# Kernel tuning notes

Measured on AMD Instinct MI355X. Metric: run time of the kernel, lower is better.

Reference implementation:

```python
import jax, jax.numpy as jnp
import numpy as np

N = 512    # nnodes
H = 8      # attention heads
C = 32     # gnn_repr_size (per head)
ER = 32    # edge_repr_size
FE = 3     # feat_emb_size
E = 16384  # edges (avg degree 32)


def gat_conv(x, edge_index, edge_attr, W, att_src, att_dst, We, att_edge, b):
    """PyG GATConv (edge_dim=1, concat=True, add_self_loops=True, eval mode)."""
    n = x.shape[0]
    h_, c_ = att_src.shape
    row, col = edge_index[0], edge_index[1]
    # self loops with fill_value='mean': mean of incoming edge_attr per target node
    deg = jax.ops.segment_sum(jnp.ones_like(edge_attr), col, num_segments=n)
    loop_attr = jax.ops.segment_sum(edge_attr, col, num_segments=n) / jnp.maximum(deg, 1.0)
    ar = jnp.arange(n)
    row = jnp.concatenate([row, ar])
    col = jnp.concatenate([col, ar])
    ea = jnp.concatenate([edge_attr, loop_attr])
    # node projections [n, H, C]
    h = (x @ W.T).reshape(n, h_, c_)
    a_src = jnp.sum(h * att_src, axis=-1)  # [n, H]
    a_dst = jnp.sum(h * att_dst, axis=-1)  # [n, H]
    e = (ea[:, None] @ We.T).reshape(-1, h_, c_)  # [E', H, C]
    a_e = jnp.sum(e * att_edge, axis=-1)          # [E', H]
    alpha = jax.nn.leaky_relu(a_src[row] + a_dst[col] + a_e, 0.2)
    # softmax over edges grouped by destination node
    amax = jax.ops.segment_max(alpha, col, num_segments=n)
    ex = jnp.exp(alpha - amax[col])
    denom = jax.ops.segment_sum(ex, col, num_segments=n)
    alpha = ex / (denom[col] + 1e-16)
    out = jax.ops.segment_sum(h[row] * alpha[..., None], col, num_segments=n)
    return out.reshape(n, h_ * c_) + b


def setup_inputs():
    key = jax.random.key(0)
    ks = jax.random.split(key, 24)
    s = 0.05
    HC = H * C
    in_len = N * ER + 3 * N + 3 * FE  # combiner1 input length
    return {
        "dist": jax.random.uniform(ks[0], (N, N), dtype=jnp.float32),
        "markov": jax.random.uniform(ks[1], (N, N), dtype=jnp.float32),
        "demand": jax.random.normal(ks[2], (N,), dtype=jnp.float32),
        "W_week": jax.random.normal(ks[3], (7, FE)) * s,
        "W_cap": jax.random.normal(ks[4], (26, FE)) * s,
        "W_veh": jax.random.normal(ks[5], (15, FE)) * s,
        "g1_W": jax.random.normal(ks[6], (HC, 1)) * s,
        "g1_att_src": jax.random.normal(ks[7], (H, C)) * s,
        "g1_att_dst": jax.random.normal(ks[8], (H, C)) * s,
        "g1_We": jax.random.normal(ks[9], (HC, 1)) * s,
        "g1_att_edge": jax.random.normal(ks[10], (H, C)) * s,
        "g1_b": jnp.zeros((HC,), dtype=jnp.float32),
        "g2_W": jax.random.normal(ks[11], (HC, HC)) * s,
        "g2_att_src": jax.random.normal(ks[12], (H, C)) * s,
        "g2_att_dst": jax.random.normal(ks[13], (H, C)) * s,
        "g2_We": jax.random.normal(ks[14], (HC, 1)) * s,
        "g2_att_edge": jax.random.normal(ks[15], (H, C)) * s,
        "g2_b": jnp.zeros((HC,), dtype=jnp.float32),
        "Wes": jax.random.normal(ks[16], (ER, 2 * HC)) * s,
        "bes": jnp.zeros((ER,), dtype=jnp.float32),
        "Wc1": jax.random.normal(ks[17], (N, in_len)) * 0.01,
        "bc1": jnp.zeros((N,), dtype=jnp.float32),
        "Wc2": jax.random.normal(ks[18], (N, N)) * s,
        "bc2": jnp.zeros((N,), dtype=jnp.float32),
        "stops": jax.random.randint(ks[19], (256,), 0, N),
        "edge_index": jax.random.randint(ks[20], (2, E), 0, N),
        "weekday": 3,
        "vehicles": 7,
        "capacity": 12,
    }


def reference(dist, markov, demand, W_week, W_cap, W_veh,
              g1_W, g1_att_src, g1_att_dst, g1_We, g1_att_edge, g1_b,
              g2_W, g2_att_src, g2_att_dst, g2_We, g2_att_edge, g2_b,
              Wes, bes, Wc1, bc1, Wc2, bc2,
              stops, edge_index, weekday, vehicles, capacity):
    n = dist.shape[0]
    dist = (dist - dist.min()) / (dist.max() - dist.min())
    x = demand[:, None]  # [n, 1]
    ea = markov[edge_index[0], edge_index[1]]  # [E]
    x = jax.nn.relu(gat_conv(x, edge_index, ea, g1_W, g1_att_src, g1_att_dst, g1_We, g1_att_edge, g1_b))
    x = jax.nn.relu(gat_conv(x, edge_index, ea, g2_W, g2_att_src, g2_att_dst, g2_We, g2_att_edge, g2_b))
    HC_ = x.shape[1]
    # all-pairs edge representation: concat(x[i], x[j]) over meshgrid -> [n*n, 2*HC]
    er = jnp.concatenate([
        jnp.broadcast_to(x[:, None, :], (n, n, HC_)),
        jnp.broadcast_to(x[None, :, :], (n, n, HC_)),
    ], axis=-1).reshape(n * n, 2 * HC_)
    er = (er @ Wes.T + bes).reshape(n, -1)  # [n, n*ER]
    week = jnp.broadcast_to(W_week[weekday], (n, W_week.shape[1]))
    cap = jnp.broadcast_to(W_cap[capacity], (n, W_cap.shape[1]))
    veh = jnp.broadcast_to(W_veh[vehicles], (n, W_veh.shape[1]))
    stop = jnp.broadcast_to(jnp.zeros((n,), dtype=dist.dtype).at[stops].set(1.0)[None, :], (n, n))
    feat = jnp.concatenate([er, dist, markov, week, cap, veh, stop], axis=1)
    out = jax.nn.relu(feat @ Wc1.T + bc1) @ Wc2.T + bc2
    return out
```

## Files before the change

### kernel.cpp

```cpp
#include <hip/hip_runtime.h>
#include <hip/hip_bf16.h>

typedef __hip_bfloat16 bf16;
typedef __attribute__((ext_vector_type(8))) short bf16x8;
typedef __attribute__((ext_vector_type(4))) float f32x4;

#define NNODE 512
#define NEDGE 16384
#define INLEN 17929
#define K1P   1088

#define WS_EA      0
#define WS_CSRC    16384
#define WS_CEA     32768
#define WS_DEG     49152
#define WS_STARTS  49664
#define WS_LATTR   50176
#define WS_MM      50688
#define WS_MMP     50690
#define WS_STOPV   50818
#define WS_AE      51330
#define WS_PS      51346
#define WS_H       55552
#define WS_G2WT    186624
#define WS_H2      317696
#define WS_ASRC    448768
#define WS_ADST    452864
#define WS_UV      456960
#define WS_K       489728
#define WS_APACK   490240
#define WS_BPACK   768768
#define WS_OUT1    1047296
#define WS_WC2B    1178368
#define WS_WESF    1309440
#define WS_ASRC2   1325824
#define WS_ADST2   1329920
#define WS_CURSOR  1334016
#define WS_DEGP    1334528
#define WS_LSUMP   1367296

static __device__ __forceinline__ unsigned short f2bfbits(float x){
  bf16 b = __float2bfloat16(x);
  union { bf16 b; unsigned short u; } c; c.b = b; return c.u;
}

__global__ __launch_bounds__(256)
void k_prep(const float* __restrict__ demand, const float* __restrict__ W1,
            const float* __restrict__ att_s, const float* __restrict__ att_d,
            const int* __restrict__ stops, const float* __restrict__ Wes,
            const float* __restrict__ dist, const float* __restrict__ markov,
            const int* __restrict__ eidx,
            const float* __restrict__ g1We, const float* __restrict__ g1ae,
            const float* __restrict__ g2We, const float* __restrict__ g2ae,
            const float* __restrict__ g2W,  const float* __restrict__ g2as,
            const float* __restrict__ g2ad, const float* __restrict__ Wc2,
            float* ws){
  int b = blockIdx.x, tid = threadIdx.x;
  if (b < 512){
    int hd = tid>>5, c = tid&31;
    float hv = demand[b] * W1[tid];
    ws[WS_H + b*256 + tid] = hv;
    float ps = hv * att_s[tid];
    float pd = hv * att_d[tid];
    for (int off=16; off; off>>=1){ ps += __shfl_down(ps,off,32); pd += __shfl_down(pd,off,32); }
    if (c==0){ ws[WS_ASRC + b*8+hd]=ps; ws[WS_ADST + b*8+hd]=pd; }
  } else if (b == 512){
    ws[WS_STOPV+tid] = 0.f; ws[WS_STOPV+256+tid] = 0.f;
    __syncthreads();
    ws[WS_STOPV + stops[tid]] = 1.0f;
    if (tid < 8){
      float s=0.f; for (int c=0;c<32;c++) s += g1We[tid*32+c]*g1ae[tid*32+c];
      ws[WS_AE+tid]=s;
    } else if (tid < 16){
      int h=tid-8; float s=0.f; for (int c=0;c<32;c++) s += g2We[h*32+c]*g2ae[h*32+c];
      ws[WS_AE+8+h]=s;
    }
  } else if (b < 515){
    for (int idx = (b-513)*8192 + tid; idx < (b-512)*8192; idx += 256){
      int k = idx>>8, c = idx&255;
      ws[WS_WESF+idx] = (k<32) ? Wes[k*512+c] : Wes[(k-32)*512+256+c];
    }
  } else if (b < 579){
    __shared__ float smn[256], smx[256];
    int p = b-515;
    float mn = 3.4e38f, mx = -3.4e38f;
    const float4* dv = (const float4*)(dist + p*4096);
    #pragma unroll
    for (int k=0;k<4;k++){
      float4 v = dv[k*256 + tid];
      mn = fminf(mn, fminf(fminf(v.x,v.y), fminf(v.z,v.w)));
      mx = fmaxf(mx, fmaxf(fmaxf(v.x,v.y), fmaxf(v.z,v.w)));
    }
    smn[tid]=mn; smx[tid]=mx; __syncthreads();
    for (int off=128; off; off>>=1){
      if (tid<off){ smn[tid]=fminf(smn[tid],smn[tid+off]); smx[tid]=fmaxf(smx[tid],smx[tid+off]); }
      __syncthreads();
    }
    if (tid==0){ ws[WS_MMP+p]=smn[0]; ws[WS_MMP+64+p]=smx[0]; }
  } else if (b < 643){
    __shared__ int   hd_[512];
    __shared__ float hf_[512];
    int k = b-579;
    hd_[tid]=0; hd_[256+tid]=0; hf_[tid]=0.f; hf_[256+tid]=0.f;
    __syncthreads();
    int e = k*256 + tid;
    int r = eidx[e], c = eidx[NEDGE+e];
    float a = markov[r*NNODE + c];
    ws[WS_EA+e] = a;
    atomicAdd(&hd_[c], 1);
    atomicAdd(&hf_[c], a);
    __syncthreads();
    ((int*)(ws+WS_DEGP))[k*512+tid]     = hd_[tid];
    ((int*)(ws+WS_DEGP))[k*512+256+tid] = hd_[256+tid];
    ws[WS_LSUMP + k*512+tid]     = hf_[tid];
    ws[WS_LSUMP + k*512+256+tid] = hf_[256+tid];
  } else if (b < 659){
    int j = b-643;
    const float* att = (j<8) ? g2as : g2ad;
    int h = j&7;
    float s = 0.f;
    for (int c=0;c<32;c++) s += att[h*32+c] * g2W[(h*32+c)*256 + tid];
    ws[WS_PS + j*256 + tid] = s;
  } else if (b < 675){
    __shared__ float T[64][65];
    int tb = b-659, tr = tb>>2, tc = tb&3;
    int w = tid>>6, c = tid&63;
    for (int k=0;k<16;k++){
      int r = k*4 + w;
      T[r][c] = g2W[(tr*64+r)*256 + tc*64 + c];
    }
    __syncthreads();
    for (int k=0;k<16;k++){
      int r = k*4 + w;
      ws[WS_G2WT + (tc*64+r)*256 + tr*64 + c] = T[c][r];
    }
  } else if (b == 675){
    ((int*)(ws+WS_CURSOR))[tid] = 0;
    ((int*)(ws+WS_CURSOR))[256+tid] = 0;
  } else {
    int blk = b - 676;
    const float4* src = (const float4*)(Wc2 + blk*4096);
    ushort4* dst = (ushort4*)((unsigned short*)(ws+WS_WC2B) + blk*4096);
    #pragma unroll
    for (int i=0;i<4;i++){
      float4 v = src[i*256+tid];
      ushort4 u;
      u.x = f2bfbits(v.x); u.y = f2bfbits(v.y);
      u.z = f2bfbits(v.z); u.w = f2bfbits(v.w);
      dst[i*256+tid] = u;
    }
  }
}

__global__ __launch_bounds__(512)
void k_scansc(const int* __restrict__ eidx, float* ws){
  __shared__ int sc[512];
  __shared__ int startS[512];
  __shared__ float rmn[64], rmx[64];
  int t = threadIdx.x, b = blockIdx.x;
  const int* dp = (const int*)(ws+WS_DEGP);
  int d = 0;
  for (int k=0;k<64;k++) d += dp[k*512+t];
  sc[t] = d; __syncthreads();
  for (int off=1; off<512; off<<=1){
    int v = (t>=off) ? sc[t-off] : 0; __syncthreads();
    sc[t] += v; __syncthreads();
  }
  startS[t] = sc[t]-d;
  if (b == 0){
    float l = 0.f;
    for (int k=0;k<64;k++) l += ws[WS_LSUMP+k*512+t];
    ((int*)(ws+WS_STARTS))[t] = startS[t];
    ((int*)(ws+WS_DEG))[t] = d;
    ws[WS_LATTR+t] = l / (float)(d>1 ? d : 1);
    if (t < 64){ rmn[t]=ws[WS_MMP+t]; rmx[t]=ws[WS_MMP+64+t]; }
    __syncthreads();
    if (t == 0){
      float mn=rmn[0], mx=rmx[0];
      for (int i=1;i<64;i++){ mn=fminf(mn,rmn[i]); mx=fmaxf(mx,rmx[i]); }
      ws[WS_MM]=mn; ws[WS_MM+1]=mx;
    }
  }
  __syncthreads();
  int e = b*512 + t;
  int c = eidx[NEDGE+e];
  int p = startS[c] + atomicAdd((int*)(ws+WS_CURSOR)+c, 1);
  ((int*)(ws+WS_CSRC))[p] = eidx[e];
  ws[WS_CEA+p] = ws[WS_EA+e];
}

template<int MODE>
__global__ __launch_bounds__(256)
void k_agg(const float* __restrict__ hbuf, const float* __restrict__ asrc,
           const float* __restrict__ adst, const int* __restrict__ csrc,
           const float* __restrict__ cea, const int* __restrict__ starts,
           const int* __restrict__ deg, const float* __restrict__ lattr,
           const float* __restrict__ AEp, const float* __restrict__ bvec,
           const float* __restrict__ dist, const float* __restrict__ markov,
           float* ws){
  int t = blockIdx.x, tid = threadIdx.x, hd = tid>>5;
  __shared__ int   srcE[256];
  __shared__ float eaE[256];
  __shared__ float Lall[256*8];
  __shared__ float AE[8], mh[8], dh[8], sw[8];
  __shared__ float xrow[256], uvrow[64];
  if (tid<8) AE[tid]=AEp[tid];
  __syncthreads();
  int d = deg[t], s0 = starts[t];
  if (d > 256) d = 256;
  for (int e=tid; e<d; e+=256){ srcE[e]=csrc[s0+e]; eaE[e]=cea[s0+e]; }
  __syncthreads();
  {
    int h8 = tid&7;
    float adt = adst[t*8+h8], aeh = AE[h8];
    for (int e = tid>>3; e < d; e += 32){
      float a = asrc[srcE[e]*8+h8] + adt + eaE[e]*aeh;
      Lall[e*8+h8] = a>=0.f ? a : 0.2f*a;
    }
  }
  __syncthreads();
  {
    int h = tid>>5, j = tid&31;
    float aself = asrc[t*8+h] + adst[t*8+h] + lattr[t]*AE[h];
    aself = aself>=0.f ? aself : 0.2f*aself;
    float mm = aself;
    for (int e=j; e<d; e+=32) mm = fmaxf(mm, Lall[e*8+h]);
    for (int off=16; off; off>>=1) mm = fmaxf(mm, __shfl_down(mm,off,32));
    mm = __shfl(mm, 0, 32);
    float dd = 0.f;
    for (int e=j; e<d; e+=32) dd += __expf(Lall[e*8+h]-mm);
    for (int off=16; off; off>>=1) dd += __shfl_down(dd,off,32);
    if (j==0){
      float se = __expf(aself-mm);
      mh[h]=mm; dh[h]=dd+se+1e-16f; sw[h]=se;
    }
  }
  __syncthreads();
  {
    int h8 = tid&7;
    for (int e = tid>>3; e < d; e += 32)
      Lall[e*8+h8] = __expf(Lall[e*8+h8] - mh[h8]);
  }
  __syncthreads();
  float a0 = sw[hd]*hbuf[t*256+tid], a1=0.f, a2=0.f, a3=0.f;
  int e = 0;
  for (; e+4<=d; e+=4){
    a0 += Lall[(e+0)*8+hd]*hbuf[srcE[e+0]*256+tid];
    a1 += Lall[(e+1)*8+hd]*hbuf[srcE[e+1]*256+tid];
    a2 += Lall[(e+2)*8+hd]*hbuf[srcE[e+2]*256+tid];
    a3 += Lall[(e+3)*8+hd]*hbuf[srcE[e+3]*256+tid];
  }
  for (; e<d; e++) a0 += Lall[e*8+hd]*hbuf[srcE[e]*256+tid];
  float v = fmaxf(((a0+a1)+(a2+a3))/dh[hd] + bvec[tid], 0.f);
  xrow[tid] = v;
  __syncthreads();
  if (MODE == 1){
    const float* g2wt = ws + WS_G2WT;
    float h0=0.f,h1=0.f,h2=0.f,h3=0.f;
    for (int c=0;c<256;c+=4){
      h0 += xrow[c+0]*g2wt[(c+0)*256+tid];
      h1 += xrow[c+1]*g2wt[(c+1)*256+tid];
      h2 += xrow[c+2]*g2wt[(c+2)*256+tid];
      h3 += xrow[c+3]*g2wt[(c+3)*256+tid];
    }
    ws[WS_H2 + t*256 + tid] = (h0+h1)+(h2+h3);
    if (tid < 64){
      int j = tid>>2, q = tid&3;
      const float* pr = ws + WS_PS + j*256 + q*64;
      const float* xr = xrow + q*64;
      float p = 0.f;
      for (int c=0;c<64;c++) p += xr[c]*pr[c];
      p += __shfl_down(p,2,4);
      p += __shfl_down(p,1,4);
      if (q==0){
        if (j<8) ws[WS_ASRC2 + t*8+j] = p;
        else     ws[WS_ADST2 + t*8+(j-8)] = p;
      }
    }
  } else {
    int k = tid>>2, q = tid&3;
    const float* wr = ws + WS_WESF + k*256 + q*64;
    const float* xr = xrow + q*64;
    float p = 0.f;
    for (int c=0;c<64;c++) p += xr[c]*wr[c];
    p += __shfl_down(p,2,4);
    p += __shfl_down(p,1,4);
    if (q==0){ ws[WS_UV + t*64+k] = p; uvrow[k] = p; }
    __syncthreads();
    float mn = ws[WS_MM], mx = ws[WS_MM+1];
    float inv = 1.0f/(mx-mn);
    bf16* ap = (bf16*)(ws+WS_APACK);
    const float* mrow = markov + t*512;
    for (int j=tid; j<K1P; j+=256){
      float v2;
      if (j<32)        v2 = uvrow[j];
      else if (j<544)  v2 = (dist[t*512 + j-32] - mn) * inv;
      else if (j<1056) v2 = mrow[j-544];
      else             v2 = 0.f;
      ap[(size_t)t*K1P + j] = __float2bfloat16(v2);
    }
  }
}

__global__ __launch_bounds__(1024)
void k_skpack(const float* __restrict__ Wc1, const float* __restrict__ bc1,
              const float* __restrict__ bes, const float* __restrict__ Wweek,
              const float* __restrict__ Wcap, const float* __restrict__ Wveh,
              const int* __restrict__ wd, const int* __restrict__ vh,
              const int* __restrict__ cp, float* ws){
  int o = blockIdx.x, tid = threadIdx.x;
  __shared__ float besf[32];
  __shared__ float red[512];
  __shared__ float red2[16];
  if (tid<32) besf[tid] = bes[tid];
  __syncthreads();
  const float* wr = Wc1 + (size_t)o*INLEN;
  bf16* bp  = (bf16*)(ws+WS_BPACK);
  float be = besf[tid&31];
  const float* uvp = ws + WS_UV + ((tid>>5)<<6) + 32 + (tid&31);
  float sP = 0.f, tP0=0.f, tP1=0.f, tP2=0.f, tP3=0.f;
  #pragma unroll
  for (int i=0;i<16;i+=4){
    float w0 = wr[tid + 1024*(i+0)];
    float w1 = wr[tid + 1024*(i+1)];
    float w2 = wr[tid + 1024*(i+2)];
    float w3 = wr[tid + 1024*(i+3)];
    float u0 = uvp[2048*(i+0)];
    float u1 = uvp[2048*(i+1)];
    float u2 = uvp[2048*(i+2)];
    float u3 = uvp[2048*(i+3)];
    sP += (w0+w1)+(w2+w3);
    tP0 += w0*(u0+be);
    tP1 += w1*(u1+be);
    tP2 += w2*(u2+be);
    tP3 += w3*(u3+be);
  }
  float tP = (tP0+tP1)+(tP2+tP3);
  if (tid < 512) tP += ws[WS_STOPV+tid] * wr[17417+tid];
  if (tid < 9){
    int g = tid/3, f = tid-g*3;
    float sv = (g==0) ? Wweek[wd[0]*3+f]
             : (g==1) ? Wcap[cp[0]*3+f]
                      : Wveh[vh[0]*3+f];
    tP += sv * wr[17408+tid];
  }
  int lane = tid&63, w = tid>>6;
  sP += __shfl_down(sP, 32, 64);
  if (lane < 32) red[w*32 + lane] = sP;
  for (int off=32; off; off>>=1) tP += __shfl_down(tP, off, 64);
  if (lane == 0) red2[w] = tP;
  __syncthreads();
  if (tid < 32){
    float s = 0.f;
    #pragma unroll
    for (int k=0;k<16;k++) s += red[k*32+tid];
    bp[(size_t)o*K1P + tid] = __float2bfloat16(s);
    bp[(size_t)o*K1P + 1056 + tid] = __float2bfloat16(0.f);
  } else if (tid == 32){
    float s = 0.f;
    #pragma unroll
    for (int k=0;k<16;k++) s += red2[k];
    ws[WS_K+o] = s + bc1[o];
  }
  bp[(size_t)o*K1P + 32 + tid] = __float2bfloat16(wr[16384+tid]);
}

template<bool RELU, bool BF16OUT>
__global__ __launch_bounds__(512)
void gemm_mfma(const bf16* __restrict__ A, const bf16* __restrict__ B,
               const float* __restrict__ bias, float* __restrict__ Cf,
               bf16* __restrict__ Cb, int M, int N, int K){
  __shared__ short Als[2][4096];
  __shared__ short Bls[2][4096];
  const int tid = threadIdx.x;
  const int bm = blockIdx.y*64, bn = blockIdx.x*64;
  const int wave = tid>>6, lane = tid&63;
  const int wm = wave>>2, wn = wave&3;
  const int r = lane&15, q = lane>>4;
  f32x4 acc[2] = {};
  const int lrow = tid>>3, lk8 = tid&7;
  const bf16* Ag = A + (size_t)(bm+lrow)*K + lk8*8;
  const bf16* Bg = B + (size_t)(bn+lrow)*K + lk8*8;
  const int sidx = ((lk8>>2)*256 + (lk8&3)*64 + lrow)*8;
  const int nk = K>>6;
  float4 av = *(const float4*)(Ag);
  float4 bv = *(const float4*)(Bg);
  *(float4*)(&Als[0][sidx]) = av;
  *(float4*)(&Bls[0][sidx]) = bv;
  __syncthreads();
  for (int kk=0; kk<nk; kk++){
    int cur = kk&1, nxt = cur^1;
    if (kk+1 < nk){
      av = *(const float4*)(Ag + (kk+1)*64);
      bv = *(const float4*)(Bg + (kk+1)*64);
    }
    #pragma unroll
    for (int kk2=0; kk2<2; kk2++){
      bf16x8 bfr = *(const bf16x8*)(&Bls[cur][(kk2*256 + q*64 + wn*16 + r)*8]);
      #pragma unroll
      for (int i=0;i<2;i++){
        bf16x8 af = *(const bf16x8*)(&Als[cur][(kk2*256 + q*64 + wm*32 + i*16 + r)*8]);
        acc[i] = __builtin_amdgcn_mfma_f32_16x16x32_bf16(af, bfr, acc[i], 0,0,0);
      }
    }
    if (kk+1 < nk){
      __syncthreads();
      *(float4*)(&Als[nxt][sidx]) = av;
      *(float4*)(&Bls[nxt][sidx]) = bv;
      __syncthreads();
    }
  }
  #pragma unroll
  for (int i=0;i<2;i++){
    int row = bm + wm*32 + i*16 + q*4;
    int col = bn + wn*16 + r;
    float bi = bias ? bias[col] : 0.f;
    #pragma unroll
    for (int g=0; g<4; g++){
      float v = acc[i][g] + bi;
      if (RELU) v = fmaxf(v, 0.f);
      if (BF16OUT) Cb[(size_t)(row+g)*N + col] = __float2bfloat16(v);
      else         Cf[(size_t)(row+g)*N + col] = v;
    }
  }
}

extern "C" void kernel_launch(void* const* d_in, const int* in_sizes, int n_in,
                              void* d_out, int out_size, void* d_ws, size_t ws_size,
                              hipStream_t stream){
  const float* dist   = (const float*)d_in[0];
  const float* markov = (const float*)d_in[1];
  const float* demand = (const float*)d_in[2];
  const float* Wweek  = (const float*)d_in[3];
  const float* Wcap   = (const float*)d_in[4];
  const float* Wveh   = (const float*)d_in[5];
  const float* g1W    = (const float*)d_in[6];
  const float* g1as   = (const float*)d_in[7];
  const float* g1ad   = (const float*)d_in[8];
  const float* g1We   = (const float*)d_in[9];
  const float* g1ae   = (const float*)d_in[10];
  const float* g1b    = (const float*)d_in[11];
  const float* g2W    = (const float*)d_in[12];
  const float* g2as   = (const float*)d_in[13];
  const float* g2ad   = (const float*)d_in[14];
  const float* g2We   = (const float*)d_in[15];
  const float* g2ae   = (const float*)d_in[16];
  const float* g2b    = (const float*)d_in[17];
  const float* Wes    = (const float*)d_in[18];
  const float* bes    = (const float*)d_in[19];
  const float* Wc1    = (const float*)d_in[20];
  const float* bc1    = (const float*)d_in[21];
  const float* Wc2    = (const float*)d_in[22];
  const float* bc2    = (const float*)d_in[23];
  const int*   stops  = (const int*)d_in[24];
  const int*   eidx   = (const int*)d_in[25];
  const int*   wd     = (const int*)d_in[26];
  const int*   vh     = (const int*)d_in[27];
  const int*   cp     = (const int*)d_in[28];
  float* out = (float*)d_out;
  float* ws = (float*)d_ws;

  const int*   csrc   = (const int*)(ws+WS_CSRC);
  const float* cea    = ws+WS_CEA;
  const int*   starts = (const int*)(ws+WS_STARTS);
  const int*   deg    = (const int*)(ws+WS_DEG);
  const float* lattr  = ws+WS_LATTR;

  k_prep<<<740,256,0,stream>>>(demand, g1W, g1as, g1ad, stops, Wes, dist, markov, eidx,
                               g1We, g1ae, g2We, g2ae, g2W, g2as, g2ad, Wc2, ws);
  k_scansc<<<32,512,0,stream>>>(eidx, ws);
  k_agg<1><<<512,256,0,stream>>>(ws+WS_H, ws+WS_ASRC, ws+WS_ADST, csrc, cea, starts, deg,
                                 lattr, ws+WS_AE, g1b, dist, markov, ws);
  k_agg<2><<<512,256,0,stream>>>(ws+WS_H2, ws+WS_ASRC2, ws+WS_ADST2, csrc, cea, starts, deg,
                                 lattr, ws+WS_AE+8, g2b, dist, markov, ws);
  k_skpack<<<512,1024,0,stream>>>(Wc1, bc1, bes, Wweek, Wcap, Wveh, wd, vh, cp, ws);
  gemm_mfma<true,true><<<dim3(8,8),512,0,stream>>>((const bf16*)(ws+WS_APACK), (const bf16*)(ws+WS_BPACK),
                                                   ws+WS_K, nullptr, (bf16*)(ws+WS_OUT1), 512, 512, K1P);
  gemm_mfma<false,false><<<dim3(8,8),512,0,stream>>>((const bf16*)(ws+WS_OUT1), (const bf16*)(ws+WS_WC2B),
                                                     bc2, out, nullptr, 512, 512, 512);
}
```

Measured before the change: 204.4 us.

## Fuse all stages into one cooperative persistent kernel with grid syncs

Merges the seven separate launches (prep, scan/scatter, two aggregation passes, skpack, two GEMMs) into a single cooperative kernel of 512 blocks of 256 threads. Stages are separated by grid.sync(), and their shared memory is overlaid in a union. The aim is to remove per-launch overhead and the gaps between kernels. In exchange, the skpack and GEMM stages are reshaped to 256-thread blocks: skpack gets a longer per-thread loop, and the GEMMs run on only 64 blocks while the rest sit idle. Each grid barrier costs time, and the whole grid must fit co-resident.

```diff
diff --git a/kernel.cpp b/kernel.cpp
--- a/kernel.cpp
+++ b/kernel.cpp
@@ -1,5 +1,8 @@
 #include <hip/hip_runtime.h>
 #include <hip/hip_bf16.h>
+#include <hip/hip_cooperative_groups.h>
+
+namespace cg = cooperative_groups;
 
 typedef __hip_bfloat16 bf16;
 typedef __attribute__((ext_vector_type(8))) short bf16x8;
@@ -44,27 +47,276 @@
   union { bf16 b; unsigned short u; } c; c.b = b; return c.u;
 }
 
-__global__ __launch_bounds__(256)
-void k_prep(const float* __restrict__ demand, const float* __restrict__ W1,
-            const float* __restrict__ att_s, const float* __restrict__ att_d,
-            const int* __restrict__ stops, const float* __restrict__ Wes,
-            const float* __restrict__ dist, const float* __restrict__ markov,
-            const int* __restrict__ eidx,
-            const float* __restrict__ g1We, const float* __restrict__ g1ae,
-            const float* __restrict__ g2We, const float* __restrict__ g2ae,
-            const float* __restrict__ g2W,  const float* __restrict__ g2as,
-            const float* __restrict__ g2ad, const float* __restrict__ Wc2,
-            float* ws){
-  int b = blockIdx.x, tid = threadIdx.x;
-  if (b < 512){
-    int hd = tid>>5, c = tid&31;
-    float hv = demand[b] * W1[tid];
+struct SMemU {
+  union {
+    struct { float smn[256], smx[256]; } mm;
+    struct { int hd[512]; float hf[512]; } hist;
+    struct { float T[64][65]; } tr;
+    struct { int a[512], bb[512]; } scan;
+    struct { int srcE[256]; float eaE[256]; float Lall[2048];
+             float AE[8], mh[8], dh[8], sw[8], xrow[256], uvrow[64]; } agg;
+    struct { float red[128], red2[4]; } sk;
+    struct { short Als[2][4096], Bls[2][4096]; } ge;
+  } u;
+};
+
+template<int MODE>
+static __device__ __forceinline__
+void agg_phase(int b, int tid, SMemU& sm,
+               const float* hbuf, const float* asrc, const float* adst,
+               const float* bvec, const float* AEp,
+               const float* dist, const float* markov, float* ws){
+  auto& A = sm.u.agg;
+  int hd = tid>>5;
+  if (tid<8) A.AE[tid]=AEp[tid];
+  __syncthreads();
+  const int* csrc = (const int*)(ws+WS_CSRC);
+  const float* cea = ws+WS_CEA;
+  int d  = ((const int*)(ws+WS_DEG))[b];
+  int s0 = ((const int*)(ws+WS_STARTS))[b];
+  if (d > 256) d = 256;
+  for (int e=tid; e<d; e+=256){ A.srcE[e]=csrc[s0+e]; A.eaE[e]=cea[s0+e]; }
+  __syncthreads();
+  {
+    int h8 = tid&7;
+    float adt = adst[b*8+h8], aeh = A.AE[h8];
+    for (int e = tid>>3; e < d; e += 32){
+      float a = asrc[A.srcE[e]*8+h8] + adt + A.eaE[e]*aeh;
+      A.Lall[e*8+h8] = a>=0.f ? a : 0.2f*a;
+    }
+  }
+  __syncthreads();
+  {
+    int h = tid>>5, j = tid&31;
+    float aself = asrc[b*8+h] + adst[b*8+h] + ws[WS_LATTR+b]*A.AE[h];
+    aself = aself>=0.f ? aself : 0.2f*aself;
+    float mm = aself;
+    for (int e=j; e<d; e+=32) mm = fmaxf(mm, A.Lall[e*8+h]);
+    for (int off=16; off; off>>=1) mm = fmaxf(mm, __shfl_down(mm,off,32));
+    mm = __shfl(mm, 0, 32);
+    float dd = 0.f;
+    for (int e=j; e<d; e+=32) dd += __expf(A.Lall[e*8+h]-mm);
+    for (int off=16; off; off>>=1) dd += __shfl_down(dd,off,32);
+    if (j==0){
+      float se = __expf(aself-mm);
+      A.mh[h]=mm; A.dh[h]=dd+se+1e-16f; A.sw[h]=se;
+    }
+  }
+  __syncthreads();
+  {
+    int h8 = tid&7;
+    for (int e = tid>>3; e < d; e += 32)
+      A.Lall[e*8+h8] = __expf(A.Lall[e*8+h8] - A.mh[h8]);
+  }
+  __syncthreads();
+  float a0 = A.sw[hd]*hbuf[b*256+tid], a1=0.f, a2=0.f, a3=0.f;
+  int e = 0;
+  for (; e+4<=d; e+=4){
+    a0 += A.Lall[(e+0)*8+hd]*hbuf[A.srcE[e+0]*256+tid];
+    a1 += A.Lall[(e+1)*8+hd]*hbuf[A.srcE[e+1]*256+tid];
+    a2 += A.Lall[(e+2)*8+hd]*hbuf[A.srcE[e+2]*256+tid];
+    a3 += A.Lall[(e+3)*8+hd]*hbuf[A.srcE[e+3]*256+tid];
+  }
+  for (; e<d; e++) a0 += A.Lall[e*8+hd]*hbuf[A.srcE[e]*256+tid];
+  float v = fmaxf(((a0+a1)+(a2+a3))/A.dh[hd] + bvec[tid], 0.f);
+  A.xrow[tid] = v;
+  __syncthreads();
+  if (MODE == 1){
+    const float* g2wt = ws + WS_G2WT;
+    float h0=0.f,h1=0.f,h2=0.f,h3=0.f;
+    for (int c=0;c<256;c+=4){
+      h0 += A.xrow[c+0]*g2wt[(c+0)*256+tid];
+      h1 += A.xrow[c+1]*g2wt[(c+1)*256+tid];
+      h2 += A.xrow[c+2]*g2wt[(c+2)*256+tid];
+      h3 += A.xrow[c+3]*g2wt[(c+3)*256+tid];
+    }
+    ws[WS_H2 + b*256 + tid] = (h0+h1)+(h2+h3);
+    if (tid < 64){
+      int j = tid>>2, q = tid&3;
+      const float* pr = ws + WS_PS + j*256 + q*64;
+      const float* xr = A.xrow + q*64;
+      float p = 0.f;
+      for (int c=0;c<64;c++) p += xr[c]*pr[c];
+      p += __shfl_down(p,2,4);
+      p += __shfl_down(p,1,4);
+      if (q==0){
+        if (j<8) ws[WS_ASRC2 + b*8+j] = p;
+        else     ws[WS_ADST2 + b*8+(j-8)] = p;
+      }
+    }
+  } else {
+    int k = tid>>2, q = tid&3;
+    const float* wrr = ws + WS_WESF + k*256 + q*64;
+    const float* xr = A.xrow + q*64;
+    float p = 0.f;
+    for (int c=0;c<64;c++) p += xr[c]*wrr[c];
+    p += __shfl_down(p,2,4);
+    p += __shfl_down(p,1,4);
+    if (q==0){ ws[WS_UV + b*64+k] = p; A.uvrow[k] = p; }
+    __syncthreads();
+    float mn = ws[WS_MM], mx = ws[WS_MM+1];
+    float inv = 1.0f/(mx-mn);
+    bf16* ap = (bf16*)(ws+WS_APACK);
+    const float* mrow = markov + b*512;
+    for (int j=tid; j<K1P; j+=256){
+      float v2;
+      if (j<32)        v2 = A.uvrow[j];
+      else if (j<544)  v2 = (dist[b*512 + j-32] - mn) * inv;
+      else if (j<1056) v2 = mrow[j-544];
+      else             v2 = 0.f;
+      ap[(size_t)b*K1P + j] = __float2bfloat16(v2);
+    }
+  }
+}
+
+template<bool RELU, bool BF16OUT>
+static __device__ __forceinline__
+void gemm_phase(int b, int tid, SMemU& sm, const bf16* A, const bf16* B,
+                const float* bias, float* Cf, bf16* Cb, int N, int K){
+  auto& G = sm.u.ge;
+  const int bm = (b>>3)*64, bn = (b&7)*64;
+  const int wave = tid>>6, lane = tid&63;
+  const int wm = wave>>1, wn = wave&1;
+  const int r = lane&15, q = lane>>4;
+  f32x4 acc[2][2] = {};
+  const int lrow = tid>>2, o0 = tid&3;
+  const bf16* Ag = A + (size_t)(bm+lrow)*K + o0*8;
+  const bf16* Bg = B + (size_t)(bn+lrow)*K + o0*8;
+  const int s0 = (o0*64 + lrow)*8, s1 = s0 + 2048;
+  const int nk = K>>6;
+  float4 a0 = *(const float4*)(Ag),    a1 = *(const float4*)(Ag+32);
+  float4 b0 = *(const float4*)(Bg),    b1 = *(const float4*)(Bg+32);
+  *(float4*)(&G.Als[0][s0]) = a0; *(float4*)(&G.Als[0][s1]) = a1;
+  *(float4*)(&G.Bls[0][s0]) = b0; *(float4*)(&G.Bls[0][s1]) = b1;
+  __syncthreads();
+  for (int kk=0; kk<nk; kk++){
+    int cur = kk&1, nxt = cur^1;
+    if (kk+1 < nk){
+      a0 = *(const float4*)(Ag + (kk+1)*64);
+      a1 = *(const float4*)(Ag + (kk+1)*64 + 32);
+      b0 = *(const float4*)(Bg + (kk+1)*64);
+      b1 = *(const float4*)(Bg + (kk+1)*64 + 32);
+    }
+    #pragma unroll
+    for (int k2=0; k2<2; k2++){
+      #pragma unroll
+      for (int j=0;j<2;j++){
+        bf16x8 bfr = *(const bf16x8*)(&G.Bls[cur][(k2*256 + q*64 + wn*32 + j*16 + r)*8]);
+        #pragma unroll
+        for (int i=0;i<2;i++){
+          bf16x8 af = *(const bf16x8*)(&G.Als[cur][(k2*256 + q*64 + wm*32 + i*16 + r)*8]);
+          acc[i][j] = __builtin_amdgcn_mfma_f32_16x16x32_bf16(af, bfr, acc[i][j], 0,0,0);
+        }
+      }
+    }
+    if (kk+1 < nk){
+      __syncthreads();
+      *(float4*)(&G.Als[nxt][s0]) = a0; *(float4*)(&G.Als[nxt][s1]) = a1;
+      *(float4*)(&G.Bls[nxt][s0]) = b0; *(float4*)(&G.Bls[nxt][s1]) = b1;
+      __syncthreads();
+    }
+  }
+  #pragma unroll
+  for (int i=0;i<2;i++){
+    int row = bm + wm*32 + i*16 + q*4;
+    #pragma unroll
+    for (int j=0;j<2;j++){
+      int col = bn + wn*32 + j*16 + r;
+      float bi = bias ? bias[col] : 0.f;
+      #pragma unroll
+      for (int g=0; g<4; g++){
+        float v = acc[i][j][g] + bi;
+        if (RELU) v = fmaxf(v, 0.f);
+        if (BF16OUT) Cb[(size_t)(row+g)*N + col] = __float2bfloat16(v);
+        else         Cf[(size_t)(row+g)*N + col] = v;
+      }
+    }
+  }
+}
+
+__global__ __launch_bounds__(256,2)
+void k_mega(const float* dist, const float* markov, const float* demand,
+            const float* Wweek, const float* Wcap, const float* Wveh,
+            const float* g1W, const float* g1as, const float* g1ad, const float* g1b,
+            const float* g1We, const float* g1ae,
+            const float* g2W, const float* g2as, const float* g2ad, const float* g2b,
+            const float* g2We, const float* g2ae,
+            const float* Wes, const float* bes,
+            const float* Wc1, const float* bc1, const float* Wc2, const float* bc2,
+            const int* stops, const int* eidx,
+            const int* wd, const int* vh, const int* cp,
+            float* out, float* ws){
+  cg::grid_group grid = cg::this_grid();
+  __shared__ SMemU sm;
+  const int b = blockIdx.x, tid = threadIdx.x;
+
+  {
+    int c = tid&31, h8 = tid>>5;
+    float hv = demand[b] * g1W[tid];
     ws[WS_H + b*256 + tid] = hv;
-    float ps = hv * att_s[tid];
-    float pd = hv * att_d[tid];
+    float ps = hv * g1as[tid];
+    float pd = hv * g1ad[tid];
     for (int off=16; off; off>>=1){ ps += __shfl_down(ps,off,32); pd += __shfl_down(pd,off,32); }
-    if (c==0){ ws[WS_ASRC + b*8+hd]=ps; ws[WS_ADST + b*8+hd]=pd; }
-  } else if (b == 512){
+    if (c==0){ ws[WS_ASRC + b*8+h8]=ps; ws[WS_ADST + b*8+h8]=pd; }
+  }
+  if (b < 64){
+    float mn = 3.4e38f, mx = -3.4e38f;
+    const float4* dv = (const float4*)(dist + b*4096);
+    #pragma unroll
+    for (int k=0;k<4;k++){
+      float4 v = dv[k*256 + tid];
+      mn = fminf(mn, fminf(fminf(v.x,v.y), fminf(v.z,v.w)));
+      mx = fmaxf(mx, fmaxf(fmaxf(v.x,v.y), fmaxf(v.z,v.w)));
+    }
+    sm.u.mm.smn[tid]=mn; sm.u.mm.smx[tid]=mx; __syncthreads();
+    for (int off=128; off; off>>=1){
+      if (tid<off){
+        sm.u.mm.smn[tid]=fminf(sm.u.mm.smn[tid],sm.u.mm.smn[tid+off]);
+        sm.u.mm.smx[tid]=fmaxf(sm.u.mm.smx[tid],sm.u.mm.smx[tid+off]);
+      }
+      __syncthreads();
+    }
+    if (tid==0){ ws[WS_MMP+b]=sm.u.mm.smn[0]; ws[WS_MMP+64+b]=sm.u.mm.smx[0]; }
+  } else if (b < 128){
+    int k = b-64;
+    sm.u.hist.hd[tid]=0; sm.u.hist.hd[256+tid]=0;
+    sm.u.hist.hf[tid]=0.f; sm.u.hist.hf[256+tid]=0.f;
+    __syncthreads();
+    int e = k*256 + tid;
+    int r = eidx[e], c = eidx[NEDGE+e];
+    float a = markov[r*NNODE + c];
+    ws[WS_EA+e] = a;
+    atomicAdd(&sm.u.hist.hd[c], 1);
+    atomicAdd(&sm.u.hist.hf[c], a);
+    __syncthreads();
+    ((int*)(ws+WS_DEGP))[k*512+tid]     = sm.u.hist.hd[tid];
+    ((int*)(ws+WS_DEGP))[k*512+256+tid] = sm.u.hist.hd[256+tid];
+    ws[WS_LSUMP + k*512+tid]     = sm.u.hist.hf[tid];
+    ws[WS_LSUMP + k*512+256+tid] = sm.u.hist.hf[256+tid];
+  } else if (b < 144){
+    int j = b-128;
+    const float* att = (j<8) ? g2as : g2ad;
+    int h = j&7;
+    float s = 0.f;
+    for (int c=0;c<32;c++) s += att[h*32+c] * g2W[(h*32+c)*256 + tid];
+    ws[WS_PS + j*256 + tid] = s;
+  } else if (b < 160){
+    int tb = b-144, tr = tb>>2, tc = tb&3;
+    int w = tid>>6, c = tid&63;
+    for (int k=0;k<16;k++){
+      int r = k*4 + w;
+      sm.u.tr.T[r][c] = g2W[(tr*64+r)*256 + tc*64 + c];
+    }
+    __syncthreads();
+    for (int k=0;k<16;k++){
+      int r = k*4 + w;
+      ws[WS_G2WT + (tc*64+r)*256 + tr*64 + c] = sm.u.tr.T[c][r];
+    }
+  } else if (b < 224){
+    int idx = (b-160)*256 + tid;
+    int k = idx>>8, c = idx&255;
+    ws[WS_WESF+idx] = (k<32) ? Wes[k*512+c] : Wes[(k-32)*512+256+c];
+  } else if (b == 224){
     ws[WS_STOPV+tid] = 0.f; ws[WS_STOPV+256+tid] = 0.f;
     __syncthreads();
     ws[WS_STOPV + stops[tid]] = 1.0f;
@@ -75,354 +327,133 @@
       int h=tid-8; float s=0.f; for (int c=0;c<32;c++) s += g2We[h*32+c]*g2ae[h*32+c];
       ws[WS_AE+8+h]=s;
     }
-  } else if (b < 515){
-    for (int idx = (b-513)*8192 + tid; idx < (b-512)*8192; idx += 256){
-      int k = idx>>8, c = idx&255;
-      ws[WS_WESF+idx] = (k<32) ? Wes[k*512+c] : Wes[(k-32)*512+256+c];
-    }
-  } else if (b < 579){
-    __shared__ float smn[256], smx[256];
-    int p = b-515;
-    float mn = 3.4e38f, mx = -3.4e38f;
-    const float4* dv = (const float4*)(dist + p*4096);
-    #pragma unroll
-    for (int k=0;k<4;k++){
-      float4 v = dv[k*256 + tid];
-      mn = fminf(mn, fminf(fminf(v.x,v.y), fminf(v.z,v.w)));
-      mx = fmaxf(mx, fmaxf(fmaxf(v.x,v.y), fmaxf(v.z,v.w)));
-    }
-    smn[tid]=mn; smx[tid]=mx; __syncthreads();
-    for (int off=128; off; off>>=1){
-      if (tid<off){ smn[tid]=fminf(smn[tid],smn[tid+off]); smx[tid]=fmaxf(smx[tid],smx[tid+off]); }
-      __syncthreads();
-    }
-    if (tid==0){ ws[WS_MMP+p]=smn[0]; ws[WS_MMP+64+p]=smx[0]; }
-  } else if (b < 643){
-    __shared__ int   hd_[512];
-    __shared__ float hf_[512];
-    int k = b-579;
-    hd_[tid]=0; hd_[256+tid]=0; hf_[tid]=0.f; hf_[256+tid]=0.f;
-    __syncthreads();
-    int e = k*256 + tid;
-    int r = eidx[e], c = eidx[NEDGE+e];
-    float a = markov[r*NNODE + c];
-    ws[WS_EA+e] = a;
-    atomicAdd(&hd_[c], 1);
-    atomicAdd(&hf_[c], a);
-    __syncthreads();
-    ((int*)(ws+WS_DEGP))[k*512+tid]     = hd_[tid];
-    ((int*)(ws+WS_DEGP))[k*512+256+tid] = hd_[256+tid];
-    ws[WS_LSUMP + k*512+tid]     = hf_[tid];
-    ws[WS_LSUMP + k*512+256+tid] = hf_[256+tid];
-  } else if (b < 659){
-    int j = b-643;
-    const float* att = (j<8) ? g2as : g2ad;
-    int h = j&7;
-    float s = 0.f;
-    for (int c=0;c<32;c++) s += att[h*32+c] * g2W[(h*32+c)*256 + tid];
-    ws[WS_PS + j*256 + tid] = s;
-  } else if (b < 675){
-    __shared__ float T[64][65];
-    int tb = b-659, tr = tb>>2, tc = tb&3;
-    int w = tid>>6, c = tid&63;
-    for (int k=0;k<16;k++){
-      int r = k*4 + w;
-      T[r][c] = g2W[(tr*64+r)*256 + tc*64 + c];
-    }
-    __syncthreads();
-    for (int k=0;k<16;k++){
-      int r = k*4 + w;
-      ws[WS_G2WT + (tc*64+r)*256 + tr*64 + c] = T[c][r];
-    }
-  } else if (b == 675){
+  } else if (b == 225){
     ((int*)(ws+WS_CURSOR))[tid] = 0;
     ((int*)(ws+WS_CURSOR))[256+tid] = 0;
-  } else {
-    int blk = b - 676;
+  } else if (b < 290){
+    int blk = b - 226;
     const float4* src = (const float4*)(Wc2 + blk*4096);
     ushort4* dst = (ushort4*)((unsigned short*)(ws+WS_WC2B) + blk*4096);
     #pragma unroll
     for (int i=0;i<4;i++){
       float4 v = src[i*256+tid];
-      ushort4 u;
-      u.x = f2bfbits(v.x); u.y = f2bfbits(v.y);
-      u.z = f2bfbits(v.z); u.w = f2bfbits(v.w);
-      dst[i*256+tid] = u;
-    }
-  }
-}
-
-__global__ __launch_bounds__(512)
-void k_scansc(const int* __restrict__ eidx, float* ws){
-  __shared__ int sc[512];
-  __shared__ int startS[512];
-  __shared__ float rmn[64], rmx[64];
-  int t = threadIdx.x, b = blockIdx.x;
-  const int* dp = (const int*)(ws+WS_DEGP);
-  int d = 0;
-  for (int k=0;k<64;k++) d += dp[k*512+t];
-  sc[t] = d; __syncthreads();
-  for (int off=1; off<512; off<<=1){
-    int v = (t>=off) ? sc[t-off] : 0; __syncthreads();
-    sc[t] += v; __syncthreads();
-  }
-  startS[t] = sc[t]-d;
+      ushort4 uu;
+      uu.x = f2bfbits(v.x); uu.y = f2bfbits(v.y);
+      uu.z = f2bfbits(v.z); uu.w = f2bfbits(v.w);
+      dst[i*256+tid] = uu;
+    }
+  }
+  grid.sync();
+
   if (b == 0){
-    float l = 0.f;
-    for (int k=0;k<64;k++) l += ws[WS_LSUMP+k*512+t];
-    ((int*)(ws+WS_STARTS))[t] = startS[t];
-    ((int*)(ws+WS_DEG))[t] = d;
-    ws[WS_LATTR+t] = l / (float)(d>1 ? d : 1);
-    if (t < 64){ rmn[t]=ws[WS_MMP+t]; rmx[t]=ws[WS_MMP+64+t]; }
-    __syncthreads();
-    if (t == 0){
-      float mn=rmn[0], mx=rmx[0];
-      for (int i=1;i<64;i++){ mn=fminf(mn,rmn[i]); mx=fmaxf(mx,rmx[i]); }
-      ws[WS_MM]=mn; ws[WS_MM+1]=mx;
-    }
-  }
-  __syncthreads();
-  int e = b*512 + t;
-  int c = eidx[NEDGE+e];
-  int p = startS[c] + atomicAdd((int*)(ws+WS_CURSOR)+c, 1);
-  ((int*)(ws+WS_CSRC))[p] = eidx[e];
-  ws[WS_CEA+p] = ws[WS_EA+e];
-}
-
-template<int MODE>
-__global__ __launch_bounds__(256)
-void k_agg(const float* __restrict__ hbuf, const float* __restrict__ asrc,
-           const float* __restrict__ adst, const int* __restrict__ csrc,
-           const float* __restrict__ cea, const int* __restrict__ starts,
-           const int* __restrict__ deg, const float* __restrict__ lattr,
-           const float* __restrict__ AEp, const float* __restrict__ bvec,
-           const float* __restrict__ dist, const float* __restrict__ markov,
-           float* ws){
-  int t = blockIdx.x, tid = threadIdx.x, hd = tid>>5;
-  __shared__ int   srcE[256];
-  __shared__ float eaE[256];
-  __shared__ float Lall[256*8];
-  __shared__ float AE[8], mh[8], dh[8], sw[8];
-  __shared__ float xrow[256], uvrow[64];
-  if (tid<8) AE[tid]=AEp[tid];
-  __syncthreads();
-  int d = deg[t], s0 = starts[t];
-  if (d > 256) d = 256;
-  for (int e=tid; e<d; e+=256){ srcE[e]=csrc[s0+e]; eaE[e]=cea[s0+e]; }
-  __syncthreads();
+    if (tid < 64){
+      float mn = ws[WS_MMP+tid], mx = ws[WS_MMP+64+tid];
+      for (int off=32; off; off>>=1){
+        mn = fminf(mn, __shfl_down(mn,off,64));
+        mx = fmaxf(mx, __shfl_down(mx,off,64));
+      }
+      if (tid==0){ ws[WS_MM]=mn; ws[WS_MM+1]=mx; }
+    }
+    const int* dp = (const int*)(ws+WS_DEGP);
+    int d0=0, d1=0; float l0=0.f, l1=0.f;
+    for (int k=0;k<64;k++){
+      d0 += dp[k*512+tid];       d1 += dp[k*512+256+tid];
+      l0 += ws[WS_LSUMP+k*512+tid]; l1 += ws[WS_LSUMP+k*512+256+tid];
+    }
+    int* sa = sm.u.scan.a; int* sb = sm.u.scan.bb;
+    sa[tid]=d0; sa[256+tid]=d1;
+    __syncthreads();
+    for (int off=1; off<512; off<<=1){
+      sb[tid]     = sa[tid]     + ((tid>=off)     ? sa[tid-off]     : 0);
+      sb[256+tid] = sa[256+tid] + ((256+tid>=off) ? sa[256+tid-off] : 0);
+      __syncthreads();
+      int* t_ = sa; sa = sb; sb = t_;
+    }
+    ((int*)(ws+WS_STARTS))[tid]     = sa[tid]-d0;
+    ((int*)(ws+WS_STARTS))[256+tid] = sa[256+tid]-d1;
+    ((int*)(ws+WS_DEG))[tid]     = d0;
+    ((int*)(ws+WS_DEG))[256+tid] = d1;
+    ws[WS_LATTR+tid]     = l0 / (float)(d0>1 ? d0 : 1);
+    ws[WS_LATTR+256+tid] = l1 / (float)(d1>1 ? d1 : 1);
+  }
+  grid.sync();
+
+  if (tid < 32){
+    int e = b*32 + tid;
+    int c = eidx[NEDGE+e];
+    int p = ((const int*)(ws+WS_STARTS))[c] + atomicAdd((int*)(ws+WS_CURSOR)+c, 1);
+    ((int*)(ws+WS_CSRC))[p] = eidx[e];
+    ws[WS_CEA+p] = ws[WS_EA+e];
+  }
+  grid.sync();
+
+  agg_phase<1>(b, tid, sm, ws+WS_H, ws+WS_ASRC, ws+WS_ADST, g1b, ws+WS_AE,
+               dist, markov, ws);
+  grid.sync();
+
+  agg_phase<2>(b, tid, sm, ws+WS_H2, ws+WS_ASRC2, ws+WS_ADST2, g2b, ws+WS_AE+8,
+               dist, markov, ws);
+  grid.sync();
+
   {
-    int h8 = tid&7;
-    float adt = adst[t*8+h8], aeh = AE[h8];
-    for (int e = tid>>3; e < d; e += 32){
-      float a = asrc[srcE[e]*8+h8] + adt + eaE[e]*aeh;
-      Lall[e*8+h8] = a>=0.f ? a : 0.2f*a;
-    }
-  }
-  __syncthreads();
-  {
-    int h = tid>>5, j = tid&31;
-    float aself = asrc[t*8+h] + adst[t*8+h] + lattr[t]*AE[h];
-    aself = aself>=0.f ? aself : 0.2f*aself;
-    float mm = aself;
-    for (int e=j; e<d; e+=32) mm = fmaxf(mm, Lall[e*8+h]);
-    for (int off=16; off; off>>=1) mm = fmaxf(mm, __shfl_down(mm,off,32));
-    mm = __shfl(mm, 0, 32);
-    float dd = 0.f;
-    for (int e=j; e<d; e+=32) dd += __expf(Lall[e*8+h]-mm);
-    for (int off=16; off; off>>=1) dd += __shfl_down(dd,off,32);
-    if (j==0){
-      float se = __expf(aself-mm);
-      mh[h]=mm; dh[h]=dd+se+1e-16f; sw[h]=se;
-    }
-  }
-  __syncthreads();
-  {
-    int h8 = tid&7;
-    for (int e = tid>>3; e < d; e += 32)
-      Lall[e*8+h8] = __expf(Lall[e*8+h8] - mh[h8]);
-  }
-  __syncthreads();
-  float a0 = sw[hd]*hbuf[t*256+tid], a1=0.f, a2=0.f, a3=0.f;
-  int e = 0;
-  for (; e+4<=d; e+=4){
-    a0 += Lall[(e+0)*8+hd]*hbuf[srcE[e+0]*256+tid];
-    a1 += Lall[(e+1)*8+hd]*hbuf[srcE[e+1]*256+tid];
-    a2 += Lall[(e+2)*8+hd]*hbuf[srcE[e+2]*256+tid];
-    a3 += Lall[(e+3)*8+hd]*hbuf[srcE[e+3]*256+tid];
-  }
-  for (; e<d; e++) a0 += Lall[e*8+hd]*hbuf[srcE[e]*256+tid];
-  float v = fmaxf(((a0+a1)+(a2+a3))/dh[hd] + bvec[tid], 0.f);
-  xrow[tid] = v;
-  __syncthreads();
-  if (MODE == 1){
-    const float* g2wt = ws + WS_G2WT;
-    float h0=0.f,h1=0.f,h2=0.f,h3=0.f;
-    for (int c=0;c<256;c+=4){
-      h0 += xrow[c+0]*g2wt[(c+0)*256+tid];
-      h1 += xrow[c+1]*g2wt[(c+1)*256+tid];
-      h2 += xrow[c+2]*g2wt[(c+2)*256+tid];
-      h3 += xrow[c+3]*g2wt[(c+3)*256+tid];
-    }
-    ws[WS_H2 + t*256 + tid] = (h0+h1)+(h2+h3);
-    if (tid < 64){
-      int j = tid>>2, q = tid&3;
-      const float* pr = ws + WS_PS + j*256 + q*64;
-      const float* xr = xrow + q*64;
-      float p = 0.f;
-      for (int c=0;c<64;c++) p += xr[c]*pr[c];
-      p += __shfl_down(p,2,4);
-      p += __shfl_down(p,1,4);
-      if (q==0){
-        if (j<8) ws[WS_ASRC2 + t*8+j] = p;
-        else     ws[WS_ADST2 + t*8+(j-8)] = p;
-      }
-    }
-  } else {
-    int k = tid>>2, q = tid&3;
-    const float* wr = ws + WS_WESF + k*256 + q*64;
-    const float* xr = xrow + q*64;
-    float p = 0.f;
-    for (int c=0;c<64;c++) p += xr[c]*wr[c];
-    p += __shfl_down(p,2,4);
-    p += __shfl_down(p,1,4);
-    if (q==0){ ws[WS_UV + t*64+k] = p; uvrow[k] = p; }
-    __syncthreads();
-    float mn = ws[WS_MM], mx = ws[WS_MM+1];
-    float inv = 1.0f/(mx-mn);
-    bf16* ap = (bf16*)(ws+WS_APACK);
-    const float* mrow = markov + t*512;
-    for (int j=tid; j<K1P; j+=256){
-      float v2;
-      if (j<32)        v2 = uvrow[j];
-      else if (j<544)  v2 = (dist[t*512 + j-32] - mn) * inv;
-      else if (j<1056) v2 = mrow[j-544];
-      else             v2 = 0.f;
-      ap[(size_t)t*K1P + j] = __float2bfloat16(v2);
-    }
-  }
-}
-
-__global__ __launch_bounds__(1024)
-void k_skpack(const float* __restrict__ Wc1, const float* __restrict__ bc1,
-              const float* __restrict__ bes, const float* __restrict__ Wweek,
-              const float* __restrict__ Wcap, const float* __restrict__ Wveh,
-              const int* __restrict__ wd, const int* __restrict__ vh,
-              const int* __restrict__ cp, float* ws){
-  int o = blockIdx.x, tid = threadIdx.x;
-  __shared__ float besf[32];
-  __shared__ float red[512];
-  __shared__ float red2[16];
-  if (tid<32) besf[tid] = bes[tid];
-  __syncthreads();
-  const float* wr = Wc1 + (size_t)o*INLEN;
-  bf16* bp  = (bf16*)(ws+WS_BPACK);
-  float be = besf[tid&31];
-  const float* uvp = ws + WS_UV + ((tid>>5)<<6) + 32 + (tid&31);
-  float sP = 0.f, tP0=0.f, tP1=0.f, tP2=0.f, tP3=0.f;
-  #pragma unroll
-  for (int i=0;i<16;i+=4){
-    float w0 = wr[tid + 1024*(i+0)];
-    float w1 = wr[tid + 1024*(i+1)];
-    float w2 = wr[tid + 1024*(i+2)];
-    float w3 = wr[tid + 1024*(i+3)];
-    float u0 = uvp[2048*(i+0)];
-    float u1 = uvp[2048*(i+1)];
-    float u2 = uvp[2048*(i+2)];
-    float u3 = uvp[2048*(i+3)];
-    sP += (w0+w1)+(w2+w3);
-    tP0 += w0*(u0+be);
-    tP1 += w1*(u1+be);
-    tP2 += w2*(u2+be);
-    tP3 += w3*(u3+be);
-  }
-  float tP = (tP0+tP1)+(tP2+tP3);
-  if (tid < 512) tP += ws[WS_STOPV+tid] * wr[17417+tid];
-  if (tid < 9){
-    int g = tid/3, f = tid-g*3;
-    float sv = (g==0) ? Wweek[wd[0]*3+f]
-             : (g==1) ? Wcap[cp[0]*3+f]
-                      : Wveh[vh[0]*3+f];
-    tP += sv * wr[17408+tid];
-  }
-  int lane = tid&63, w = tid>>6;
-  sP += __shfl_down(sP, 32, 64);
-  if (lane < 32) red[w*32 + lane] = sP;
-  for (int off=32; off; off>>=1) tP += __shfl_down(tP, off, 64);
-  if (lane == 0) red2[w] = tP;
-  __syncthreads();
-  if (tid < 32){
-    float s = 0.f;
+    const float* wr = Wc1 + (size_t)b*INLEN;
+    bf16* bp = (bf16*)(ws+WS_BPACK);
+    float be = bes[tid&31];
+    const float* uvp = ws + WS_UV + ((tid>>5)<<6) + 32 + (tid&31);
+    float sP = 0.f, t0=0.f, t1=0.f, t2=0.f, t3=0.f;
+    for (int i=0;i<64;i+=4){
+      float w0 = wr[tid + 256*(i+0)];
+      float w1 = wr[tid + 256*(i+1)];
+      float w2 = wr[tid + 256*(i+2)];
+      float w3 = wr[tid + 256*(i+3)];
+      float u0 = uvp[512*(i+0)];
+      float u1 = uvp[512*(i+1)];
+      float u2 = uvp[512*(i+2)];
+      float u3 = uvp[512*(i+3)];
+      sP += (w0+w1)+(w2+w3);
+      t0 += w0*(u0+be);
+      t1 += w1*(u1+be);
+      t2 += w2*(u2+be);
+      t3 += w3*(u3+be);
+    }
+    float tP = (t0+t1)+(t2+t3);
+    tP += ws[WS_STOPV+tid]*wr[17417+tid] + ws[WS_STOPV+256+tid]*wr[17417+256+tid];
+    if (tid < 9){
+      int g = tid/3, f = tid-g*3;
+      float sv = (g==0) ? Wweek[wd[0]*3+f]
+               : (g==1) ? Wcap[cp[0]*3+f]
+                        : Wveh[vh[0]*3+f];
+      tP += sv * wr[17408+tid];
+    }
+    int lane = tid&63, w = tid>>6;
+    sP += __shfl_down(sP, 32, 64);
+    for (int off=32; off; off>>=1) tP += __shfl_down(tP, off, 64);
+    if (lane < 32) sm.u.sk.red[w*32+lane] = sP;
+    if (lane == 0) sm.u.sk.red2[w] = tP;
+    __syncthreads();
+    if (tid < 32){
+      float s = sm.u.sk.red[tid] + sm.u.sk.red[32+tid]
+              + sm.u.sk.red[64+tid] + sm.u.sk.red[96+tid];
+      bp[(size_t)b*K1P + tid] = __float2bfloat16(s);
+      bp[(size_t)b*K1P + 1056 + tid] = __float2bfloat16(0.f);
+    } else if (tid == 32){
+      float s = sm.u.sk.red2[0]+sm.u.sk.red2[1]+sm.u.sk.red2[2]+sm.u.sk.red2[3];
+      ws[WS_K+b] = s + bc1[b];
+    }
     #pragma unroll
-    for (int k=0;k<16;k++) s += red[k*32+tid];
-    bp[(size_t)o*K1P + tid] = __float2bfloat16(s);
-    bp[(size_t)o*K1P + 1056 + tid] = __float2bfloat16(0.f);
-  } else if (tid == 32){
-    float s = 0.f;
-    #pragma unroll
-    for (int k=0;k<16;k++) s += red2[k];
-    ws[WS_K+o] = s + bc1[o];
-  }
-  bp[(size_t)o*K1P + 32 + tid] = __float2bfloat16(wr[16384+tid]);
-}
-
-template<bool RELU, bool BF16OUT>
-__global__ __launch_bounds__(512)
-void gemm_mfma(const bf16* __restrict__ A, const bf16* __restrict__ B,
-               const float* __restrict__ bias, float* __restrict__ Cf,
-               bf16* __restrict__ Cb, int M, int N, int K){
-  __shared__ short Als[2][4096];
-  __shared__ short Bls[2][4096];
-  const int tid = threadIdx.x;
-  const int bm = blockIdx.y*64, bn = blockIdx.x*64;
-  const int wave = tid>>6, lane = tid&63;
-  const int wm = wave>>2, wn = wave&3;
-  const int r = lane&15, q = lane>>4;
-  f32x4 acc[2] = {};
-  const int lrow = tid>>3, lk8 = tid&7;
-  const bf16* Ag = A + (size_t)(bm+lrow)*K + lk8*8;
-  const bf16* Bg = B + (size_t)(bn+lrow)*K + lk8*8;
-  const int sidx = ((lk8>>2)*256 + (lk8&3)*64 + lrow)*8;
-  const int nk = K>>6;
-  float4 av = *(const float4*)(Ag);
-  float4 bv = *(const float4*)(Bg);
-  *(float4*)(&Als[0][sidx]) = av;
-  *(float4*)(&Bls[0][sidx]) = bv;
-  __syncthreads();
-  for (int kk=0; kk<nk; kk++){
-    int cur = kk&1, nxt = cur^1;
-    if (kk+1 < nk){
-      av = *(const float4*)(Ag + (kk+1)*64);
-      bv = *(const float4*)(Bg + (kk+1)*64);
-    }
-    #pragma unroll
-    for (int kk2=0; kk2<2; kk2++){
-      bf16x8 bfr = *(const bf16x8*)(&Bls[cur][(kk2*256 + q*64 + wn*16 + r)*8]);
-      #pragma unroll
-      for (int i=0;i<2;i++){
-        bf16x8 af = *(const bf16x8*)(&Als[cur][(kk2*256 + q*64 + wm*32 + i*16 + r)*8]);
-        acc[i] = __builtin_amdgcn_mfma_f32_16x16x32_bf16(af, bfr, acc[i], 0,0,0);
-      }
-    }
-    if (kk+1 < nk){
-      __syncthreads();
-      *(float4*)(&Als[nxt][sidx]) = av;
-      *(float4*)(&Bls[nxt][sidx]) = bv;
-      __syncthreads();
-    }
-  }
-  #pragma unroll
-  for (int i=0;i<2;i++){
-    int row = bm + wm*32 + i*16 + q*4;
-    int col = bn + wn*16 + r;
-    float bi = bias ? bias[col] : 0.f;
-    #pragma unroll
-    for (int g=0; g<4; g++){
-      float v = acc[i][g] + bi;
-      if (RELU) v = fmaxf(v, 0.f);
-      if (BF16OUT) Cb[(size_t)(row+g)*N + col] = __float2bfloat16(v);
-      else         Cf[(size_t)(row+g)*N + col] = v;
-    }
-  }
+    for (int qq=0; qq<4; qq++)
+      bp[(size_t)b*K1P + 32 + tid + 256*qq] = __float2bfloat16(wr[16384 + tid + 256*qq]);
+  }
+  grid.sync();
+
+  if (b < 64)
+    gemm_phase<true,true>(b, tid, sm, (const bf16*)(ws+WS_APACK), (const bf16*)(ws+WS_BPACK),
+                          ws+WS_K, nullptr, (bf16*)(ws+WS_OUT1), 512, K1P);
+  grid.sync();
+
+  if (b < 64)
+    gemm_phase<false,false>(b, tid, sm, (const bf16*)(ws+WS_OUT1), (const bf16*)(ws+WS_WC2B),
+                            bc2, out, nullptr, 512, 512);
 }
 
 extern "C" void kernel_launch(void* const* d_in, const int* in_sizes, int n_in,
@@ -458,24 +489,20 @@
   const int*   vh     = (const int*)d_in[27];
   const int*   cp     = (const int*)d_in[28];
   float* out = (float*)d_out;
-  float* ws = (float*)d_ws;
-
-  const int*   csrc   = (const int*)(ws+WS_CSRC);
-  const float* cea    = ws+WS_CEA;
-  const int*   starts = (const int*)(ws+WS_STARTS);
-  const int*   deg    = (const int*)(ws+WS_DEG);
-  const float* lattr  = ws+WS_LATTR;
-
-  k_prep<<<740,256,0,stream>>>(demand, g1W, g1as, g1ad, stops, Wes, dist, markov, eidx,
-                               g1We, g1ae, g2We, g2ae, g2W, g2as, g2ad, Wc2, ws);
-  k_scansc<<<32,512,0,stream>>>(eidx, ws);
-  k_agg<1><<<512,256,0,stream>>>(ws+WS_H, ws+WS_ASRC, ws+WS_ADST, csrc, cea, starts, deg,
-                                 lattr, ws+WS_AE, g1b, dist, markov, ws);
-  k_agg<2><<<512,256,0,stream>>>(ws+WS_H2, ws+WS_ASRC2, ws+WS_ADST2, csrc, cea, starts, deg,
-                                 lattr, ws+WS_AE+8, g2b, dist, markov, ws);
-  k_skpack<<<512,1024,0,stream>>>(Wc1, bc1, bes, Wweek, Wcap, Wveh, wd, vh, cp, ws);
-  gemm_mfma<true,true><<<dim3(8,8),512,0,stream>>>((const bf16*)(ws+WS_APACK), (const bf16*)(ws+WS_BPACK),
-                                                   ws+WS_K, nullptr, (bf16*)(ws+WS_OUT1), 512, 512, K1P);
-  gemm_mfma<false,false><<<dim3(8,8),512,0,stream>>>((const bf16*)(ws+WS_OUT1), (const bf16*)(ws+WS_WC2B),
-                                                     bc2, out, nullptr, 512, 512, 512);
+  float* ws  = (float*)d_ws;
+
+  void* args[] = {
+    (void*)&dist, (void*)&markov, (void*)&demand,
+    (void*)&Wweek, (void*)&Wcap, (void*)&Wveh,
+    (void*)&g1W, (void*)&g1as, (void*)&g1ad, (void*)&g1b,
+    (void*)&g1We, (void*)&g1ae,
+    (void*)&g2W, (void*)&g2as, (void*)&g2ad, (void*)&g2b,
+    (void*)&g2We, (void*)&g2ae,
+    (void*)&Wes, (void*)&bes,
+    (void*)&Wc1, (void*)&bc1, (void*)&Wc2, (void*)&bc2,
+    (void*)&stops, (void*)&eidx,
+    (void*)&wd, (void*)&vh, (void*)&cp,
+    (void*)&out, (void*)&ws
+  };
+  hipLaunchCooperativeKernel((const void*)k_mega, dim3(512), dim3(256), args, 0, stream);
 }
```

Result: slower. 626.4 us (+206.4%).
